# Performance work log

Hardware: AMD Instinct MI355X
Metric: run time of the kernel (lower is better)

## Reference

```python
import jax, jax.numpy as jnp
import numpy as np

N = 100000
E = 3200000
IN_FEAT = 128
OUT_FEAT = 128


def setup_inputs() -> dict:
    key = jax.random.key(0)
    k1, k2, k3, k4, k5, k6 = jax.random.split(key, 6)
    x = jax.random.normal(k1, (N, IN_FEAT), dtype=jnp.float32)
    edge_row = jax.random.randint(k2, (E,), 0, N, dtype=jnp.int32)
    edge_col = jax.random.randint(k3, (E,), 0, N, dtype=jnp.int32)
    edge_weight = jax.random.uniform(k4, (E,), dtype=jnp.float32)
    # nn.Linear(in_feat, out_feat) params
    bound = 1.0 / np.sqrt(IN_FEAT)
    W = jax.random.uniform(k5, (OUT_FEAT, IN_FEAT), dtype=jnp.float32, minval=-bound, maxval=bound)
    b = jax.random.uniform(k6, (OUT_FEAT,), dtype=jnp.float32, minval=-bound, maxval=bound)
    return {"x": x, "edge_row": edge_row, "edge_col": edge_col,
            "edge_weight": edge_weight, "W": W, "b": b, "k": 4}


def _spmm(edge_row, edge_col, edge_weight, x):
    # sparse adj (COO) @ dense x : gather source rows, scale, scatter-add to dest rows
    msgs = edge_weight[:, None] * x[edge_col]          # [E, F]
    return jax.ops.segment_sum(msgs, edge_row, num_segments=N)


def reference(x, edge_row, edge_col, edge_weight, W, b, k):
    for _ in range(k):
        x = _spmm(edge_row, edge_col, edge_weight, x)  # [N, F]
    # nn.Linear: x @ W^T + b
    return x @ W.T + b
```

## Files before the change

### kernel.cpp

```cpp
#include <hip/hip_runtime.h>
#include <hip/hip_fp16.h>


#define F 128
#define CH 2048
#define MAXB 256
#define RB_LOG 9
#define RB (1 << RB_LOG)
#define CAPB 18432

typedef _Float16 half8 __attribute__((ext_vector_type(8)));
typedef float f32x4 __attribute__((ext_vector_type(4)));

__global__ void zero_i32(int* __restrict__ p, int n) {
  int i = blockIdx.x * blockDim.x + threadIdx.x;
  if (i < n) p[i] = 0;
}

__global__ __launch_bounds__(256) void bucket_scatter(
    const int* __restrict__ erow, const int* __restrict__ ecol,
    const float* __restrict__ ew, int* __restrict__ bcnt,
    int2* __restrict__ mid, int e, int nb) {
  __shared__ int2 stage[CH];
  __shared__ unsigned short sbid[CH];
  __shared__ int cnt[MAXB], lstart[MAXB], gbase[MAXB], cnt2[MAXB];
  int tid = threadIdx.x;
  int base = blockIdx.x * CH;
  for (int t = tid; t < nb; t += 256) { cnt[t] = 0; cnt2[t] = 0; }
  __syncthreads();
  for (int j = tid; j < CH; j += 256) {
    int i = base + j;
    if (i < e) atomicAdd(&cnt[erow[i] >> RB_LOG], 1);
  }
  __syncthreads();
  if (tid == 0) {
    int run = 0;
    for (int t = 0; t < nb; ++t) { lstart[t] = run; run += cnt[t]; }
  }
  __syncthreads();
  for (int t = tid; t < nb; t += 256)
    if (cnt[t] > 0) gbase[t] = atomicAdd(&bcnt[t], cnt[t]);
  __syncthreads();
  for (int j = tid; j < CH; j += 256) {
    int i = base + j;
    if (i < e) {
      int r = erow[i];
      int bb = r >> RB_LOG;
      int k = atomicAdd(&cnt2[bb], 1);
      int p = lstart[bb] + k;
      stage[p] = make_int2(((r & (RB - 1)) << 17) | ecol[i], __float_as_int(ew[i]));
      sbid[p] = (unsigned short)bb;
    }
  }
  __syncthreads();
  int tot = e - base; if (tot > CH) tot = CH;
  for (int j = tid; j < tot; j += 256) {
    int bb = sbid[j];
    mid[(size_t)bb * CAPB + gbase[bb] + (j - lstart[bb])] = stage[j];
  }
}

__global__ __launch_bounds__(256) void bscan(const int* __restrict__ bcnt,
                                             int* __restrict__ bbase, int nb) {
  __shared__ int ps[256];
  int t = threadIdx.x;
  int v = (t < nb) ? bcnt[t] : 0;
  ps[t] = v;
  __syncthreads();
  for (int off = 1; off < 256; off <<= 1) {
    int u = (t >= off) ? ps[t - off] : 0;
    __syncthreads();
    ps[t] += u;
    __syncthreads();
  }
  if (t < nb) bbase[t] = ps[t] - v;
  if (t == nb - 1) bbase[nb] = ps[t];
}

__global__ __launch_bounds__(256) void csr_sort(
    const int2* __restrict__ mid, const int* __restrict__ bcnt,
    const int* __restrict__ bbase, int* __restrict__ rptr,
    int2* __restrict__ edges, int n, int nb) {
  __shared__ int rcnt[RB];
  __shared__ int rofs[RB];
  __shared__ int psum[256];
  __shared__ int2 st[CAPB];
  int b = blockIdx.x, tid = threadIdx.x;
  int r0 = b << RB_LOG;
  int r1 = r0 + RB; if (r1 > n) r1 = n;
  int nr = r1 - r0;
  int cnt  = bcnt[b];
  int base = bbase[b];
  const int2* src = mid + (size_t)b * CAPB;

  for (int r = tid; r < RB; r += 256) rcnt[r] = 0;
  __syncthreads();
  for (int i = tid; i < cnt; i += 256)
    atomicAdd(&rcnt[((unsigned)src[i].x) >> 17], 1);
  __syncthreads();
  int s2 = rcnt[2 * tid] + rcnt[2 * tid + 1];
  psum[tid] = s2;
  __syncthreads();
  for (int off = 1; off < 256; off <<= 1) {
    int u = (tid >= off) ? psum[tid - off] : 0;
    __syncthreads();
    psum[tid] += u;
    __syncthreads();
  }
  int ex = (tid > 0) ? psum[tid - 1] : 0;
  rofs[2 * tid]     = ex;
  rofs[2 * tid + 1] = ex + rcnt[2 * tid];
  __syncthreads();
  for (int r = tid; r < nr; r += 256) rptr[r0 + r] = base + rofs[r];
  if (b == nb - 1 && tid == 0) rptr[n] = base + cnt;
  for (int i = tid; i < cnt; i += 256) {
    int2 ed = src[i];
    int rl  = ((unsigned)ed.x) >> 17;
    int col = ed.x & 0x1FFFF;
    int p = atomicAdd(&rofs[rl], 1);
    st[p] = make_int2(col, ed.y);
  }
  __syncthreads();
  for (int i = tid; i < cnt; i += 256) edges[base + i] = st[i];
}

__global__ __launch_bounds__(256) void spmm_kernel(
    const int* __restrict__ rptr, const int2* __restrict__ edges,
    const __half* __restrict__ xin, __half* __restrict__ xout, int n) {
  int lane = threadIdx.x & 63;
  int hid = lane >> 5;
  int fl  = lane & 31;
  int row = (blockIdx.x << 2) + (threadIdx.x >> 6);
  if (row >= n) return;
  int s = rptr[row], e = rptr[row + 1];
  float4 acc = make_float4(0.f, 0.f, 0.f, 0.f);
  const char* xb = (const char*)xin;

#define GATHER_FMA(ED)                                                        \
  {                                                                           \
    float w = __int_as_float((ED).y);                                         \
    short4 hv = *(const short4*)(xb + ((size_t)(ED).x << 8) + (fl << 3));     \
    union { short2 s2; __half2 h2; } u0, u1;                                  \
    u0.s2 = make_short2(hv.x, hv.y);                                          \
    u1.s2 = make_short2(hv.z, hv.w);                                          \
    float2 f0 = __half22float2(u0.h2);                                        \
    float2 f1 = __half22float2(u1.h2);                                        \
    acc.x = fmaf(w, f0.x, acc.x); acc.y = fmaf(w, f0.y, acc.y);               \
    acc.z = fmaf(w, f1.x, acc.z); acc.w = fmaf(w, f1.y, acc.w);               \
  }

  int i = s;
  for (; i + 7 < e; i += 8) {
    int4 p0 = *(const int4*)&edges[i];
    int4 p1 = *(const int4*)&edges[i + 2];
    int4 p2 = *(const int4*)&edges[i + 4];
    int4 p3 = *(const int4*)&edges[i + 6];
    int2 e0 = hid ? make_int2(p0.z, p0.w) : make_int2(p0.x, p0.y);
    int2 e1 = hid ? make_int2(p1.z, p1.w) : make_int2(p1.x, p1.y);
    int2 e2 = hid ? make_int2(p2.z, p2.w) : make_int2(p2.x, p2.y);
    int2 e3 = hid ? make_int2(p3.z, p3.w) : make_int2(p3.x, p3.y);
    GATHER_FMA(e0); GATHER_FMA(e1); GATHER_FMA(e2); GATHER_FMA(e3);
  }
  for (; i + 1 < e; i += 2) {
    int4 p0 = *(const int4*)&edges[i];
    int2 e0 = hid ? make_int2(p0.z, p0.w) : make_int2(p0.x, p0.y);
    GATHER_FMA(e0);
  }
  if (i < e && hid == 0) {
    int2 e0 = edges[i];
    GATHER_FMA(e0);
  }
#undef GATHER_FMA

  acc.x += __shfl_xor(acc.x, 32, 64);
  acc.y += __shfl_xor(acc.y, 32, 64);
  acc.z += __shfl_xor(acc.z, 32, 64);
  acc.w += __shfl_xor(acc.w, 32, 64);
  if (hid == 0) {
    union { short4 s4; __half2 h2[2]; } o;
    o.h2[0] = __float22half2_rn(make_float2(acc.x, acc.y));
    o.h2[1] = __float22half2_rn(make_float2(acc.z, acc.w));
    *(short4*)((char*)xout + ((size_t)row << 8) + (fl << 3)) = o.s4;
  }
}

__global__ void f32_to_f16(const float2* __restrict__ in, __half2* __restrict__ out, int n2) {
  int i = blockIdx.x * blockDim.x + threadIdx.x;
  if (i < n2) out[i] = __float22half2_rn(in[i]);
}

__global__ __launch_bounds__(256) void linear_mfma(
    const __half* __restrict__ xin, const __half* __restrict__ Wh,
    const float* __restrict__ b, float* __restrict__ out, int n) {
  int lane = threadIdx.x & 63;
  int wv   = threadIdx.x >> 6;
  int rbase = blockIdx.x * 64 + wv * 16;
  if (rbase >= n) return;
  int arow = rbase + (lane & 15);
  if (arow >= n) arow = n - 1;
  int koff = (lane >> 4) * 8;

  half8 a0 = *(const half8*)(xin + (size_t)arow * F + 0  + koff);
  half8 a1 = *(const half8*)(xin + (size_t)arow * F + 32 + koff);
  half8 a2 = *(const half8*)(xin + (size_t)arow * F + 64 + koff);
  half8 a3 = *(const half8*)(xin + (size_t)arow * F + 96 + koff);

  int drow0 = rbase + (lane >> 4) * 4;
  int dcol  = lane & 15;
#pragma unroll
  for (int jt = 0; jt < 8; ++jt) {
    const __half* wrow = Wh + (size_t)(jt * 16 + (lane & 15)) * F + koff;
    half8 b0 = *(const half8*)(wrow + 0);
    half8 b1 = *(const half8*)(wrow + 32);
    half8 b2 = *(const half8*)(wrow + 64);
    half8 b3 = *(const half8*)(wrow + 96);
    f32x4 acc = {0.f, 0.f, 0.f, 0.f};
    acc = __builtin_amdgcn_mfma_f32_16x16x32_f16(a0, b0, acc, 0, 0, 0);
    acc = __builtin_amdgcn_mfma_f32_16x16x32_f16(a1, b1, acc, 0, 0, 0);
    acc = __builtin_amdgcn_mfma_f32_16x16x32_f16(a2, b2, acc, 0, 0, 0);
    acc = __builtin_amdgcn_mfma_f32_16x16x32_f16(a3, b3, acc, 0, 0, 0);
    float bias = b[jt * 16 + dcol];
#pragma unroll
    for (int m = 0; m < 4; ++m) {
      int r = drow0 + m;
      if (r < n) out[(size_t)r * F + jt * 16 + dcol] = acc[m] + bias;
    }
  }
}

__global__ void w_to_f16(const float* __restrict__ W, __half* __restrict__ Wh, int n) {
  int i = blockIdx.x * blockDim.x + threadIdx.x;
  if (i < n) Wh[i] = __float2half(W[i]);
}

extern "C" void kernel_launch(void* const* d_in, const int* in_sizes, int n_in,
                              void* d_out, int out_size, void* d_ws, size_t ws_size,
                              hipStream_t stream) {
  const float* x    = (const float*)d_in[0];
  const int*   erow = (const int*)d_in[1];
  const int*   ecol = (const int*)d_in[2];
  const float* ew   = (const float*)d_in[3];
  const float* W    = (const float*)d_in[4];
  const float* b    = (const float*)d_in[5];
  float* out = (float*)d_out;

  const int N = in_sizes[0] / F;
  const int E = in_sizes[1];

  char* ws = (char*)d_ws;
  size_t off = 0;
  int2*  edges  = (int2*)(ws + off);   off += (size_t)E * 8;
  int*   rptr   = (int*)(ws + off);    off += (size_t)(N + 1) * 4;
  int*   bcnt   = (int*)(ws + off);    off += MAXB * 4;
  int*   bbase  = (int*)(ws + off);    off += (MAXB + 1) * 4;
  off = (off + 255) & ~(size_t)255;
  __half* Wh    = (__half*)(ws + off); off += (size_t)F * F * 2;
  off = (off + 255) & ~(size_t)255;
  __half2* bufA = (__half2*)(ws + off);
  __half2* bufB = (__half2*)(ws + off + (size_t)N * F * 2);
  int2*    mid  = (int2*)bufA;

  const int BK = 256;
  int nb = (N + RB - 1) >> RB_LOG;

  zero_i32<<<1, 256, 0, stream>>>(bcnt, nb);
  bucket_scatter<<<(E + CH - 1) / CH, 256, 0, stream>>>(erow, ecol, ew, bcnt, mid, E, nb);
  bscan<<<1, 256, 0, stream>>>(bcnt, bbase, nb);
  csr_sort<<<nb, 256, 0, stream>>>(mid, bcnt, bbase, rptr, edges, N, nb);

  w_to_f16<<<(F * F + BK - 1) / BK, BK, 0, stream>>>(W, Wh, F * F);
  int n2 = N * (F / 2);
  f32_to_f16<<<(n2 + BK - 1) / BK, BK, 0, stream>>>((const float2*)x, bufB, n2);
  int spmm_grid = (N + 3) / 4;
  spmm_kernel<<<spmm_grid, 256, 0, stream>>>(rptr, edges, (const __half*)bufB, (__half*)bufA, N);
  spmm_kernel<<<spmm_grid, 256, 0, stream>>>(rptr, edges, (const __half*)bufA, (__half*)bufB, N);
  spmm_kernel<<<spmm_grid, 256, 0, stream>>>(rptr, edges, (const __half*)bufB, (__half*)bufA, N);
  spmm_kernel<<<spmm_grid, 256, 0, stream>>>(rptr, edges, (const __half*)bufA, (__half*)bufB, N);

  linear_mfma<<<(N + 63) / 64, 256, 0, stream>>>((const __half*)bufB, Wh, b, out, N);
}
```

Before: 591.3 us.

## Merge setup launches, fold bucket scan into CSR sort, pre-shift column offsets

Merges the bcnt-zeroing and W conversion into one prep kernel. The separate bucket scan kernel is removed: each csr_sort block now reduces the bucket counts before its own bucket. bucket_scatter caches edges in shared memory so they are read from global once, and uses a parallel scan for local offsets. The SpMM kernel gets pre-shifted byte offsets, per-lane int2 edge loads, two accumulators for more ILP, and a launch_bounds occupancy hint. This reduces launch count and integer work, but adds shared-memory use in bucket_scatter (lower occupancy) and redundant reductions in csr_sort.

Measured after the change: 589.3 us. About the same (-0.3%).

```diff
diff --git a/kernel.cpp b/kernel.cpp
--- a/kernel.cpp
+++ b/kernel.cpp
@@ -12,75 +12,73 @@
 typedef _Float16 half8 __attribute__((ext_vector_type(8)));
 typedef float f32x4 __attribute__((ext_vector_type(4)));
 
-__global__ void zero_i32(int* __restrict__ p, int n) {
-  int i = blockIdx.x * blockDim.x + threadIdx.x;
-  if (i < n) p[i] = 0;
+__global__ void prep_kernel(const float* __restrict__ W, __half* __restrict__ Wh,
+                            int nw, int* __restrict__ bcnt, int nwb) {
+  int blk = blockIdx.x;
+  if (blk == nwb) {
+    int t = threadIdx.x;
+    if (t < MAXB) bcnt[t] = 0;
+  } else {
+    int i = blk * 256 + threadIdx.x;
+    if (i < nw) Wh[i] = __float2half(W[i]);
+  }
 }
 
 __global__ __launch_bounds__(256) void bucket_scatter(
     const int* __restrict__ erow, const int* __restrict__ ecol,
     const float* __restrict__ ew, int* __restrict__ bcnt,
     int2* __restrict__ mid, int e, int nb) {
+  __shared__ int  rowv[CH];
+  __shared__ int2 cw[CH];
   __shared__ int2 stage[CH];
   __shared__ unsigned short sbid[CH];
   __shared__ int cnt[MAXB], lstart[MAXB], gbase[MAXB], cnt2[MAXB];
+  __shared__ int ps[256];
   int tid = threadIdx.x;
   int base = blockIdx.x * CH;
+  int tot = e - base; if (tot > CH) tot = CH;
   for (int t = tid; t < nb; t += 256) { cnt[t] = 0; cnt2[t] = 0; }
   __syncthreads();
-  for (int j = tid; j < CH; j += 256) {
+  for (int j = tid; j < tot; j += 256) {
     int i = base + j;
-    if (i < e) atomicAdd(&cnt[erow[i] >> RB_LOG], 1);
-  }
-  __syncthreads();
-  if (tid == 0) {
-    int run = 0;
-    for (int t = 0; t < nb; ++t) { lstart[t] = run; run += cnt[t]; }
-  }
+    int r = erow[i];
+    rowv[j] = r;
+    cw[j] = make_int2(ecol[i], __float_as_int(ew[i]));
+    atomicAdd(&cnt[r >> RB_LOG], 1);
+  }
+  __syncthreads();
+  int v = (tid < nb) ? cnt[tid] : 0;
+  ps[tid] = v;
+  __syncthreads();
+  for (int off = 1; off < 256; off <<= 1) {
+    int u = (tid >= off) ? ps[tid - off] : 0;
+    __syncthreads();
+    ps[tid] += u;
+    __syncthreads();
+  }
+  if (tid < nb) lstart[tid] = ps[tid] - v;
   __syncthreads();
   for (int t = tid; t < nb; t += 256)
     if (cnt[t] > 0) gbase[t] = atomicAdd(&bcnt[t], cnt[t]);
   __syncthreads();
-  for (int j = tid; j < CH; j += 256) {
-    int i = base + j;
-    if (i < e) {
-      int r = erow[i];
-      int bb = r >> RB_LOG;
-      int k = atomicAdd(&cnt2[bb], 1);
-      int p = lstart[bb] + k;
-      stage[p] = make_int2(((r & (RB - 1)) << 17) | ecol[i], __float_as_int(ew[i]));
-      sbid[p] = (unsigned short)bb;
-    }
-  }
-  __syncthreads();
-  int tot = e - base; if (tot > CH) tot = CH;
+  for (int j = tid; j < tot; j += 256) {
+    int r = rowv[j];
+    int bb = r >> RB_LOG;
+    int k = atomicAdd(&cnt2[bb], 1);
+    int p = lstart[bb] + k;
+    stage[p] = make_int2(((r & (RB - 1)) << 17) | cw[j].x, cw[j].y);
+    sbid[p] = (unsigned short)bb;
+  }
+  __syncthreads();
   for (int j = tid; j < tot; j += 256) {
     int bb = sbid[j];
     mid[(size_t)bb * CAPB + gbase[bb] + (j - lstart[bb])] = stage[j];
   }
 }
 
-__global__ __launch_bounds__(256) void bscan(const int* __restrict__ bcnt,
-                                             int* __restrict__ bbase, int nb) {
-  __shared__ int ps[256];
-  int t = threadIdx.x;
-  int v = (t < nb) ? bcnt[t] : 0;
-  ps[t] = v;
-  __syncthreads();
-  for (int off = 1; off < 256; off <<= 1) {
-    int u = (t >= off) ? ps[t - off] : 0;
-    __syncthreads();
-    ps[t] += u;
-    __syncthreads();
-  }
-  if (t < nb) bbase[t] = ps[t] - v;
-  if (t == nb - 1) bbase[nb] = ps[t];
-}
-
 __global__ __launch_bounds__(256) void csr_sort(
     const int2* __restrict__ mid, const int* __restrict__ bcnt,
-    const int* __restrict__ bbase, int* __restrict__ rptr,
-    int2* __restrict__ edges, int n, int nb) {
+    int* __restrict__ rptr, int2* __restrict__ edges, int n, int nb) {
   __shared__ int rcnt[RB];
   __shared__ int rofs[RB];
   __shared__ int psum[256];
@@ -89,9 +87,17 @@
   int r0 = b << RB_LOG;
   int r1 = r0 + RB; if (r1 > n) r1 = n;
   int nr = r1 - r0;
-  int cnt  = bcnt[b];
-  int base = bbase[b];
+  int cnt = bcnt[b];
   const int2* src = mid + (size_t)b * CAPB;
+
+  psum[tid] = (tid < b && tid < nb) ? bcnt[tid] : 0;
+  __syncthreads();
+  for (int off = 128; off > 0; off >>= 1) {
+    if (tid < off) psum[tid] += psum[tid + off];
+    __syncthreads();
+  }
+  int bas = psum[0];
+  __syncthreads();
 
   for (int r = tid; r < RB; r += 256) rcnt[r] = 0;
   __syncthreads();
@@ -111,20 +117,20 @@
   rofs[2 * tid]     = ex;
   rofs[2 * tid + 1] = ex + rcnt[2 * tid];
   __syncthreads();
-  for (int r = tid; r < nr; r += 256) rptr[r0 + r] = base + rofs[r];
-  if (b == nb - 1 && tid == 0) rptr[n] = base + cnt;
+  for (int r = tid; r < nr; r += 256) rptr[r0 + r] = bas + rofs[r];
+  if (b == nb - 1 && tid == 0) rptr[n] = bas + cnt;
   for (int i = tid; i < cnt; i += 256) {
     int2 ed = src[i];
     int rl  = ((unsigned)ed.x) >> 17;
     int col = ed.x & 0x1FFFF;
     int p = atomicAdd(&rofs[rl], 1);
-    st[p] = make_int2(col, ed.y);
-  }
-  __syncthreads();
-  for (int i = tid; i < cnt; i += 256) edges[base + i] = st[i];
-}
-
-__global__ __launch_bounds__(256) void spmm_kernel(
+    st[p] = make_int2(col << 8, ed.y);
+  }
+  __syncthreads();
+  for (int i = tid; i < cnt; i += 256) edges[bas + i] = st[i];
+}
+
+__global__ __launch_bounds__(256, 8) void spmm_kernel(
     const int* __restrict__ rptr, const int2* __restrict__ edges,
     const __half* __restrict__ xin, __half* __restrict__ xout, int n) {
   int lane = threadIdx.x & 63;
@@ -134,44 +140,42 @@
   if (row >= n) return;
   int s = rptr[row], e = rptr[row + 1];
   float4 acc = make_float4(0.f, 0.f, 0.f, 0.f);
+  float4 ac2 = make_float4(0.f, 0.f, 0.f, 0.f);
   const char* xb = (const char*)xin;
 
-#define GATHER_FMA(ED)                                                        \
+#define GATHER_FMA(ED, A)                                                     \
   {                                                                           \
     float w = __int_as_float((ED).y);                                         \
-    short4 hv = *(const short4*)(xb + ((size_t)(ED).x << 8) + (fl << 3));     \
+    short4 hv = *(const short4*)(xb + (size_t)(unsigned)(ED).x + (fl << 3));  \
     union { short2 s2; __half2 h2; } u0, u1;                                  \
     u0.s2 = make_short2(hv.x, hv.y);                                          \
     u1.s2 = make_short2(hv.z, hv.w);                                          \
     float2 f0 = __half22float2(u0.h2);                                        \
     float2 f1 = __half22float2(u1.h2);                                        \
-    acc.x = fmaf(w, f0.x, acc.x); acc.y = fmaf(w, f0.y, acc.y);               \
-    acc.z = fmaf(w, f1.x, acc.z); acc.w = fmaf(w, f1.y, acc.w);               \
+    A.x = fmaf(w, f0.x, A.x); A.y = fmaf(w, f0.y, A.y);                       \
+    A.z = fmaf(w, f1.x, A.z); A.w = fmaf(w, f1.y, A.w);                       \
   }
 
   int i = s;
   for (; i + 7 < e; i += 8) {
-    int4 p0 = *(const int4*)&edges[i];
-    int4 p1 = *(const int4*)&edges[i + 2];
-    int4 p2 = *(const int4*)&edges[i + 4];
-    int4 p3 = *(const int4*)&edges[i + 6];
-    int2 e0 = hid ? make_int2(p0.z, p0.w) : make_int2(p0.x, p0.y);
-    int2 e1 = hid ? make_int2(p1.z, p1.w) : make_int2(p1.x, p1.y);
-    int2 e2 = hid ? make_int2(p2.z, p2.w) : make_int2(p2.x, p2.y);
-    int2 e3 = hid ? make_int2(p3.z, p3.w) : make_int2(p3.x, p3.y);
-    GATHER_FMA(e0); GATHER_FMA(e1); GATHER_FMA(e2); GATHER_FMA(e3);
+    int2 e0 = edges[i + hid];
+    int2 e1 = edges[i + 2 + hid];
+    int2 e2 = edges[i + 4 + hid];
+    int2 e3 = edges[i + 6 + hid];
+    GATHER_FMA(e0, acc); GATHER_FMA(e1, ac2);
+    GATHER_FMA(e2, acc); GATHER_FMA(e3, ac2);
   }
   for (; i + 1 < e; i += 2) {
-    int4 p0 = *(const int4*)&edges[i];
-    int2 e0 = hid ? make_int2(p0.z, p0.w) : make_int2(p0.x, p0.y);
-    GATHER_FMA(e0);
+    int2 e0 = edges[i + hid];
+    GATHER_FMA(e0, acc);
   }
   if (i < e && hid == 0) {
     int2 e0 = edges[i];
-    GATHER_FMA(e0);
+    GATHER_FMA(e0, acc);
   }
 #undef GATHER_FMA
 
+  acc.x += ac2.x; acc.y += ac2.y; acc.z += ac2.z; acc.w += ac2.w;
   acc.x += __shfl_xor(acc.x, 32, 64);
   acc.y += __shfl_xor(acc.y, 32, 64);
   acc.z += __shfl_xor(acc.z, 32, 64);
@@ -228,11 +232,6 @@
   }
 }
 
-__global__ void w_to_f16(const float* __restrict__ W, __half* __restrict__ Wh, int n) {
-  int i = blockIdx.x * blockDim.x + threadIdx.x;
-  if (i < n) Wh[i] = __float2half(W[i]);
-}
-
 extern "C" void kernel_launch(void* const* d_in, const int* in_sizes, int n_in,
                               void* d_out, int out_size, void* d_ws, size_t ws_size,
                               hipStream_t stream) {
@@ -252,7 +251,6 @@
   int2*  edges  = (int2*)(ws + off);   off += (size_t)E * 8;
   int*   rptr   = (int*)(ws + off);    off += (size_t)(N + 1) * 4;
   int*   bcnt   = (int*)(ws + off);    off += MAXB * 4;
-  int*   bbase  = (int*)(ws + off);    off += (MAXB + 1) * 4;
   off = (off + 255) & ~(size_t)255;
   __half* Wh    = (__half*)(ws + off); off += (size_t)F * F * 2;
   off = (off + 255) & ~(size_t)255;
@@ -262,13 +260,12 @@
 
   const int BK = 256;
   int nb = (N + RB - 1) >> RB_LOG;
-
-  zero_i32<<<1, 256, 0, stream>>>(bcnt, nb);
+  int nwb = (F * F + BK - 1) / BK;
+
+  prep_kernel<<<nwb + 1, BK, 0, stream>>>(W, Wh, F * F, bcnt, nwb);
   bucket_scatter<<<(E + CH - 1) / CH, 256, 0, stream>>>(erow, ecol, ew, bcnt, mid, E, nb);
-  bscan<<<1, 256, 0, stream>>>(bcnt, bbase, nb);
-  csr_sort<<<nb, 256, 0, stream>>>(mid, bcnt, bbase, rptr, edges, N, nb);
-
-  w_to_f16<<<(F * F + BK - 1) / BK, BK, 0, stream>>>(W, Wh, F * F);
+  csr_sort<<<nb, 256, 0, stream>>>(mid, bcnt, rptr, edges, N, nb);
+
   int n2 = N * (F / 2);
   f32_to_f16<<<(n2 + BK - 1) / BK, BK, 0, stream>>>((const float2*)x, bufB, n2);
   int spmm_grid = (N + 3) / 4;
```
